# Optimization experiments

Measured on AMD Instinct MI355X. Metric: run time of the kernel, lower is better.

The kernel has to match this reference:

```python
import jax, jax.numpy as jnp
import numpy as np


def _sobel_weights():
    # ImageGradientsLayer: fixed Sobel x/y filters, shape (O=2, I=1, 3, 3)
    gx = jnp.array([[-1., 0., 1.], [-2., 0., 2.], [-1., 0., 1.]], dtype=jnp.float32)
    gy = jnp.array([[-1., -2., -1.], [0., 0., 0.], [1., 2., 1.]], dtype=jnp.float32)
    return jnp.stack([gx, gy])[:, None, :, :]


def _orientation_weights():
    # SIFTOrientationLayer: 8 unit orientation vectors + 2x2 identity, shape (10, 2)
    ratios = jnp.arange(0.125, 2.125, 0.25, dtype=jnp.float32)  # 8 values
    ang = ratios * jnp.pi
    vec = jnp.stack([jnp.cos(ang), jnp.sin(ang)], axis=1)  # (8, 2)
    return jnp.concatenate([vec, jnp.eye(2, dtype=jnp.float32)], axis=0)  # (10, 2)


def setup_inputs() -> dict:
    key = jax.random.key(0)
    x = jax.random.normal(key, (8, 1, 1024, 1024), dtype=jnp.float32)
    return {"x": x, "sobel_w": _sobel_weights(), "orient_w": _orientation_weights()}


def reference(x, sobel_w, orient_w):
    # 1) ImageGradientsLayer: 3x3 Sobel conv, padding=1 -> (B, 2, H, W)
    grads = jax.lax.conv_general_dilated(
        x, sobel_w, window_strides=(1, 1), padding=((1, 1), (1, 1)),
        dimension_numbers=("NCHW", "OIHW", "NCHW"))
    # 2) SIFTOrientationLayer: 1x1 conv == channel projection -> (B, 10, H, W)
    proj = jnp.einsum("bchw,oc->bohw", grads, orient_w)
    # 3) HistogramLayer: one-hot(argmax of orientation dots) * gradient magnitude
    cosines = proj[:, :8]          # (B, 8, H, W)
    im_grads = proj[:, 8:]         # (B, 2, H, W) == grads (identity rows)
    magnitudes = jnp.sqrt(jnp.sum(im_grads * im_grads, axis=1))  # (B, H, W)
    max_idx = jnp.argmax(cosines, axis=1)                        # (B, H, W)
    onehot = jax.nn.one_hot(max_idx, 8, axis=1, dtype=x.dtype)   # (B, 8, H, W)
    hist = onehot * magnitudes[:, None, :, :]
    # 4) SubGridAccumulationLayer: depthwise 4x4 all-ones conv, pad 2 -> (B, 8, H+1, W+1)
    ones_k = jnp.ones((8, 1, 4, 4), dtype=x.dtype)
    out = jax.lax.conv_general_dilated(
        hist, ones_k, window_strides=(1, 1), padding=((2, 2), (2, 2)),
        dimension_numbers=("NCHW", "OIHW", "NCHW"), feature_group_count=8)
    return out
```

## Files before the change

kernel.cpp:

```cpp
#include <hip/hip_runtime.h>
#include <math.h>


#define TWC 61
#define WTH 16
#define WPB 4
#define BTH (WPB*WTH)
#define XC 66
#define XR (BTH+5)
#define PLANE 1050625
#define NCT 17
#define NRT 17

__global__ __launch_bounds__(256, 5)
void sift_fused(const float* __restrict__ x,
                const float* __restrict__ ow,
                float* __restrict__ out)
{
    __shared__ float sx[XR * XC];

    const int tid  = threadIdx.x;
    const int lane = tid & 63;
    const int wv   = tid >> 6;

    const int flat = blockIdx.x + NCT * (blockIdx.y + NRT * blockIdx.z);
    const int bb = flat & 7;
    const int t  = flat >> 3;
    const int bx = t % NCT;
    const int by = t / NCT;

    const int j0 = bx * TWC;
    const int r0 = by * BTH;

    const float* xb = x + (size_t)bb * 1024 * 1024;
    for (int p = tid; p < XR * XC; p += 256) {
        int r = p / XC, c = p - r * XC;
        int gr = r0 - 3 + r, gc = j0 - 3 + c;
        float v = 0.0f;
        if ((unsigned)gr < 1024u && (unsigned)gc < 1024u)
            v = xb[(size_t)gr * 1024 + gc];
        sx[p] = v;
    }
    __syncthreads();

    const int rbase = r0 + WTH * wv;
    if (rbase > 1024) return;

    float wcn[8], wsn[8];
    #pragma unroll
    for (int o = 0; o < 8; ++o) { wcn[o] = ow[2*o]; wsn[o] = ow[2*o+1]; }

    const int gcol = j0 - 2 + lane;
    const bool colok = (unsigned)gcol < 1024u;
    const int gj = j0 + lane;
    const bool canstore = (lane < TWC) && (gj <= 1024);

    float* po[8];
    #pragma unroll
    for (int o = 0; o < 8; ++o) po[o] = out + (size_t)(bb * 8 + o) * PLANE;

    const float* px = sx + (WTH * wv) * XC + lane;
    int hrow = rbase - 2;
    int orow = rbase;
    int vo   = rbase * 1025 + gj;

    float dd0, dd1, dd2, dd3, ww0, ww1, ww2, ww3;
    float cA[8], cB[8], PP0[8], PP1[8], PP2[8], PP3[8];

#define XROWLOAD(DD, WW) { \
    float n0 = px[0], n1 = px[1], n2 = px[2]; px += XC; \
    DD = n2 - n0; \
    WW = n0 + 2.0f*n1 + n2; \
}

#define HSTEP(DT, DM, DB, WT, WB, CP, CC, PR, PC, DOP, DOFIN) { \
    XROWLOAD(DB, WB) \
    float gx = DT + 2.0f*DM + DB; \
    float gy = WB - WT; \
    float msq = gx*gx + gy*gy; \
    float m = (colok && (unsigned)hrow < 1024u) \
                ? __builtin_amdgcn_sqrtf(msq) : 0.0f; \
    hrow++; \
    float pj0 = gx*wcn[0] + gy*wsn[0]; \
    float pj1 = gx*wcn[1] + gy*wsn[1]; \
    float pj2 = gx*wcn[2] + gy*wsn[2]; \
    float pj3 = gx*wcn[3] + gy*wsn[3]; \
    float pj4 = gx*wcn[4] + gy*wsn[4]; \
    float pj5 = gx*wcn[5] + gy*wsn[5]; \
    float pj6 = gx*wcn[6] + gy*wsn[6]; \
    float pj7 = gx*wcn[7] + gy*wsn[7]; \
    bool g01 = pj1 > pj0; float b01 = g01 ? pj1 : pj0; int i01 = g01 ? 1 : 0; \
    bool g23 = pj3 > pj2; float b23 = g23 ? pj3 : pj2; int i23 = g23 ? 3 : 2; \
    bool g45 = pj5 > pj4; float b45 = g45 ? pj5 : pj4; int i45 = g45 ? 5 : 4; \
    bool g67 = pj7 > pj6; float b67 = g67 ? pj7 : pj6; int i67 = g67 ? 7 : 6; \
    bool gA = b23 > b01; float bA = gA ? b23 : b01; int iA = gA ? i23 : i01; \
    bool gB = b67 > b45; float bB = gB ? b67 : b45; int iB = gB ? i67 : i45; \
    int idx = (bB > bA) ? iB : iA; \
    _Pragma("unroll") \
    for (int o = 0; o < 8; ++o) CC[o] = (idx == o) ? m : 0.0f; \
    if (DOP) { \
        _Pragma("unroll") \
        for (int o = 0; o < 8; ++o) PC[o] = CP[o] + CC[o]; \
    } \
    if (DOFIN) { \
        bool ok = canstore && (orow <= 1024); \
        _Pragma("unroll") \
        for (int o = 0; o < 8; ++o) { \
            float v = PR[o] + PC[o]; \
            v += __shfl_down(v, 1); \
            v += __shfl_down(v, 2); \
            if (ok) po[o][vo] = v; \
        } \
        vo += 1025; orow++; \
    } \
}

    XROWLOAD(dd0, ww0)
    XROWLOAD(dd1, ww1)
    HSTEP(dd0, dd1, dd2, ww0, ww2, cA, cB, PP0, PP0, 0, 0)
    HSTEP(dd1, dd2, dd3, ww1, ww3, cB, cA, PP0, PP1, 1, 0)
    HSTEP(dd2, dd3, dd0, ww2, ww0, cA, cB, PP0, PP2, 1, 0)

    #pragma unroll 1
    for (int it = 0; it < 4; ++it) {
        HSTEP(dd3, dd0, dd1, ww3, ww1, cB, cA, PP1, PP3, 1, 1)
        HSTEP(dd0, dd1, dd2, ww0, ww2, cA, cB, PP2, PP0, 1, 1)
        HSTEP(dd1, dd2, dd3, ww1, ww3, cB, cA, PP3, PP1, 1, 1)
        HSTEP(dd2, dd3, dd0, ww2, ww0, cA, cB, PP0, PP2, 1, 1)
    }

#undef HSTEP
#undef XROWLOAD
}

extern "C" void kernel_launch(void* const* d_in, const int* in_sizes, int n_in,
                              void* d_out, int out_size, void* d_ws, size_t ws_size,
                              hipStream_t stream)
{
    const float* x  = (const float*)d_in[0];
    const float* ow = (const float*)d_in[2];
    float* out = (float*)d_out;

    dim3 grid(NCT,
              NRT,
              8);
    sift_fused<<<grid, 256, 0, stream>>>(x, ow, out);
}
```

Before: 90.25 us.

## Process two columns per lane, drop LDS staging, load input directly

Each lane now computes two adjacent output columns, so a block covers 124 columns instead of 61 and fewer column tiles are launched. The shared-memory staging and its barrier are removed; each lane reads four clamped and masked input values per row directly from global memory. The argmax indices are packed into one int, and the 4x4 box sum is built from per-row one-hot magnitudes with fewer shuffles. On even rows the two outputs are written as one float2 store. This trades LDS traffic and sync for redundant global loads through cache, plus higher register pressure (launch bounds lowered to 4).

```diff
diff --git a/kernel.cpp b/kernel.cpp
--- a/kernel.cpp
+++ b/kernel.cpp
@@ -2,23 +2,18 @@
 #include <math.h>
 
 
-#define TWC 61
+#define TWC 124
 #define WTH 16
-#define WPB 4
-#define BTH (WPB*WTH)
-#define XC 66
-#define XR (BTH+5)
+#define BTH 64
+#define NCT 9
+#define NRT 17
 #define PLANE 1050625
-#define NCT 17
-#define NRT 17
 
-__global__ __launch_bounds__(256, 5)
+__global__ __launch_bounds__(256, 4)
 void sift_fused(const float* __restrict__ x,
                 const float* __restrict__ ow,
                 float* __restrict__ out)
 {
-    __shared__ float sx[XR * XC];
-
     const int tid  = threadIdx.x;
     const int lane = tid & 63;
     const int wv   = tid >> 6;
@@ -28,121 +23,173 @@
     const int t  = flat >> 3;
     const int bx = t % NCT;
     const int by = t / NCT;
-
     const int j0 = bx * TWC;
     const int r0 = by * BTH;
 
-    const float* xb = x + (size_t)bb * 1024 * 1024;
-    for (int p = tid; p < XR * XC; p += 256) {
-        int r = p / XC, c = p - r * XC;
-        int gr = r0 - 3 + r, gc = j0 - 3 + c;
-        float v = 0.0f;
-        if ((unsigned)gr < 1024u && (unsigned)gc < 1024u)
-            v = xb[(size_t)gr * 1024 + gc];
-        sx[p] = v;
-    }
-    __syncthreads();
-
     const int rbase = r0 + WTH * wv;
     if (rbase > 1024) return;
+
+    const float* xb = x + (size_t)bb * 1024 * 1024;
 
     float wcn[8], wsn[8];
     #pragma unroll
     for (int o = 0; o < 8; ++o) { wcn[o] = ow[2*o]; wsn[o] = ow[2*o+1]; }
 
-    const int gcol = j0 - 2 + lane;
-    const bool colok = (unsigned)gcol < 1024u;
-    const int gj = j0 + lane;
-    const bool canstore = (lane < TWC) && (gj <= 1024);
+    const int c0 = j0 - 3 + 2 * lane;
+    const int cc0 = min(max(c0    , 0), 1023);
+    const int cc1 = min(max(c0 + 1, 0), 1023);
+    const int cc2 = min(max(c0 + 2, 0), 1023);
+    const int cc3 = min(max(c0 + 3, 0), 1023);
+    const float mk0 = ((unsigned)(c0    ) < 1024u) ? 1.0f : 0.0f;
+    const float mk1 = ((unsigned)(c0 + 1) < 1024u) ? 1.0f : 0.0f;
+    const float mk2 = ((unsigned)(c0 + 2) < 1024u) ? 1.0f : 0.0f;
+    const float mk3 = ((unsigned)(c0 + 3) < 1024u) ? 1.0f : 0.0f;
+
+    const int h0 = j0 - 2 + 2 * lane;
+    const float cm0 = ((unsigned)h0       < 1024u) ? 1.0f : 0.0f;
+    const float cm1 = ((unsigned)(h0 + 1) < 1024u) ? 1.0f : 0.0f;
+
+    const int oc0 = j0 + 2 * lane;
+    const bool st0 = (2 * lane     < TWC) && (oc0     <= 1024);
+    const bool st1 = (2 * lane + 1 < TWC) && (oc0 + 1 <= 1024);
+    const bool stpair  = st0 && st1;
+    const bool st0only = st0 && !st1;
 
     float* po[8];
     #pragma unroll
     for (int o = 0; o < 8; ++o) po[o] = out + (size_t)(bb * 8 + o) * PLANE;
 
-    const float* px = sx + (WTH * wv) * XC + lane;
-    int hrow = rbase - 2;
+    int vo   = rbase * 1025 + oc0;
     int orow = rbase;
-    int vo   = rbase * 1025 + gj;
+    int gr   = rbase - 3;
 
-    float dd0, dd1, dd2, dd3, ww0, ww1, ww2, ww3;
-    float cA[8], cB[8], PP0[8], PP1[8], PP2[8], PP3[8];
+    float q0d0,q0d1,q0w0,q0w1, q1d0,q1d1,q1w0,q1w1;
+    float q2d0,q2d1,q2w0,q2w1, q3d0,q3d1,q3w0,q3w1;
+    float r0m0,r0m1, r1m0,r1m1, r2m0,r2m1, r3m0,r3m1;
+    int   r0ip, r1ip, r2ip, r3ip;
 
-#define XROWLOAD(DD, WW) { \
-    float n0 = px[0], n1 = px[1], n2 = px[2]; px += XC; \
-    DD = n2 - n0; \
-    WW = n0 + 2.0f*n1 + n2; \
+#define XLOAD(BD0,BD1,BW0,BW1) { \
+    float x0_,x1_,x2_,x3_; \
+    if ((unsigned)gr < 1024u) { \
+        const float* rp = xb + ((size_t)(unsigned)gr << 10); \
+        x0_ = rp[cc0]*mk0; x1_ = rp[cc1]*mk1; \
+        x2_ = rp[cc2]*mk2; x3_ = rp[cc3]*mk3; \
+    } else { x0_=0.0f; x1_=0.0f; x2_=0.0f; x3_=0.0f; } \
+    gr++; \
+    BD0 = x2_ - x0_; \
+    BD1 = x3_ - x1_; \
+    BW0 = x0_ + 2.0f*x1_ + x2_; \
+    BW1 = x1_ + 2.0f*x2_ + x3_; \
 }
 
-#define HSTEP(DT, DM, DB, WT, WB, CP, CC, PR, PC, DOP, DOFIN) { \
-    XROWLOAD(DB, WB) \
-    float gx = DT + 2.0f*DM + DB; \
-    float gy = WB - WT; \
-    float msq = gx*gx + gy*gy; \
-    float m = (colok && (unsigned)hrow < 1024u) \
-                ? __builtin_amdgcn_sqrtf(msq) : 0.0f; \
-    hrow++; \
-    float pj0 = gx*wcn[0] + gy*wsn[0]; \
-    float pj1 = gx*wcn[1] + gy*wsn[1]; \
-    float pj2 = gx*wcn[2] + gy*wsn[2]; \
-    float pj3 = gx*wcn[3] + gy*wsn[3]; \
-    float pj4 = gx*wcn[4] + gy*wsn[4]; \
-    float pj5 = gx*wcn[5] + gy*wsn[5]; \
-    float pj6 = gx*wcn[6] + gy*wsn[6]; \
-    float pj7 = gx*wcn[7] + gy*wsn[7]; \
+#define TOURN8(RES, GX, GY) { \
+    float pj0 = (GX)*wcn[0] + (GY)*wsn[0]; \
+    float pj1 = (GX)*wcn[1] + (GY)*wsn[1]; \
+    float pj2 = (GX)*wcn[2] + (GY)*wsn[2]; \
+    float pj3 = (GX)*wcn[3] + (GY)*wsn[3]; \
+    float pj4 = (GX)*wcn[4] + (GY)*wsn[4]; \
+    float pj5 = (GX)*wcn[5] + (GY)*wsn[5]; \
+    float pj6 = (GX)*wcn[6] + (GY)*wsn[6]; \
+    float pj7 = (GX)*wcn[7] + (GY)*wsn[7]; \
     bool g01 = pj1 > pj0; float b01 = g01 ? pj1 : pj0; int i01 = g01 ? 1 : 0; \
     bool g23 = pj3 > pj2; float b23 = g23 ? pj3 : pj2; int i23 = g23 ? 3 : 2; \
     bool g45 = pj5 > pj4; float b45 = g45 ? pj5 : pj4; int i45 = g45 ? 5 : 4; \
     bool g67 = pj7 > pj6; float b67 = g67 ? pj7 : pj6; int i67 = g67 ? 7 : 6; \
     bool gA = b23 > b01; float bA = gA ? b23 : b01; int iA = gA ? i23 : i01; \
     bool gB = b67 > b45; float bB = gB ? b67 : b45; int iB = gB ? i67 : i45; \
-    int idx = (bB > bA) ? iB : iA; \
-    _Pragma("unroll") \
-    for (int o = 0; o < 8; ++o) CC[o] = (idx == o) ? m : 0.0f; \
-    if (DOP) { \
-        _Pragma("unroll") \
-        for (int o = 0; o < 8; ++o) PC[o] = CP[o] + CC[o]; \
-    } \
-    if (DOFIN) { \
-        bool ok = canstore && (orow <= 1024); \
-        _Pragma("unroll") \
-        for (int o = 0; o < 8; ++o) { \
-            float v = PR[o] + PC[o]; \
-            v += __shfl_down(v, 1); \
-            v += __shfl_down(v, 2); \
-            if (ok) po[o][vo] = v; \
-        } \
-        vo += 1025; orow++; \
-    } \
+    RES = (bB > bA) ? iB : iA; \
 }
 
-    XROWLOAD(dd0, ww0)
-    XROWLOAD(dd1, ww1)
-    HSTEP(dd0, dd1, dd2, ww0, ww2, cA, cB, PP0, PP0, 0, 0)
-    HSTEP(dd1, dd2, dd3, ww1, ww3, cB, cA, PP0, PP1, 1, 0)
-    HSTEP(dd2, dd3, dd0, ww2, ww0, cA, cB, PP0, PP2, 1, 0)
+#define HSTEP(TD0,TD1,TW0,TW1, MD0,MD1,MW0,MW1, BD0,BD1,BW0,BW1, RM0,RM1,RIP) { \
+    XLOAD(BD0,BD1,BW0,BW1) \
+    float rowm = ((unsigned)(gr - 3) < 1022u) ? 1.0f : \
+                 (((unsigned)(gr - 2) < 1024u) ? 1.0f : 0.0f); \
+    rowm = ((unsigned)(gr - 2) < 1024u) ? 1.0f : 0.0f; \
+    float gm0 = cm0 * rowm, gm1 = cm1 * rowm; \
+    float gx0 = TD0 + 2.0f*MD0 + BD0; \
+    float gy0 = BW0 - TW0; \
+    float gx1 = TD1 + 2.0f*MD1 + BD1; \
+    float gy1 = BW1 - TW1; \
+    RM0 = __builtin_amdgcn_sqrtf(gx0*gx0 + gy0*gy0) * gm0; \
+    RM1 = __builtin_amdgcn_sqrtf(gx1*gx1 + gy1*gy1) * gm1; \
+    int i0_, i1_; \
+    TOURN8(i0_, gx0, gy0) \
+    TOURN8(i1_, gx1, gy1) \
+    RIP = i0_ | (i1_ << 3); \
+}
+
+#define FIN(EVENK) { \
+    bool rowok = (orow <= 1024); \
+    int e00 = r0ip & 7, e01 = r0ip >> 3; \
+    int e10 = r1ip & 7, e11 = r1ip >> 3; \
+    int e20 = r2ip & 7, e21 = r2ip >> 3; \
+    int e30 = r3ip & 7, e31 = r3ip >> 3; \
+    _Pragma("unroll") \
+    for (int o = 0; o < 8; ++o) { \
+        float a_ = (e00 == o ? r0m0 : 0.0f); \
+        a_ += (e10 == o ? r1m0 : 0.0f); \
+        a_ += (e20 == o ? r2m0 : 0.0f); \
+        a_ += (e30 == o ? r3m0 : 0.0f); \
+        float b_ = (e01 == o ? r0m1 : 0.0f); \
+        b_ += (e11 == o ? r1m1 : 0.0f); \
+        b_ += (e21 == o ? r2m1 : 0.0f); \
+        b_ += (e31 == o ? r3m1 : 0.0f); \
+        float S_ = a_ + b_; \
+        float Sd_ = __shfl_down(S_, 1); \
+        float Ad_ = __shfl_down(a_, 2); \
+        float E_ = S_ + Sd_; \
+        float O_ = b_ + Sd_ + Ad_; \
+        if (EVENK) { \
+            if (rowok && stpair) { \
+                float2 pv; pv.x = E_; pv.y = O_; \
+                *reinterpret_cast<float2*>(po[o] + vo) = pv; \
+            } else if (rowok && st0only) { \
+                po[o][vo] = E_; \
+            } \
+        } else { \
+            if (rowok && st0) po[o][vo] = E_; \
+            if (rowok && st1) po[o][vo + 1] = O_; \
+        } \
+    } \
+    vo += 1025; orow++; \
+}
+
+    XLOAD(q0d0,q0d1,q0w0,q0w1)
+    XLOAD(q1d0,q1d1,q1w0,q1w1)
+    HSTEP(q0d0,q0d1,q0w0,q0w1, q1d0,q1d1,q1w0,q1w1, q2d0,q2d1,q2w0,q2w1,
+          r0m0,r0m1,r0ip)
+    HSTEP(q1d0,q1d1,q1w0,q1w1, q2d0,q2d1,q2w0,q2w1, q3d0,q3d1,q3w0,q3w1,
+          r1m0,r1m1,r1ip)
+    HSTEP(q2d0,q2d1,q2w0,q2w1, q3d0,q3d1,q3w0,q3w1, q0d0,q0d1,q0w0,q0w1,
+          r2m0,r2m1,r2ip)
 
     #pragma unroll 1
     for (int it = 0; it < 4; ++it) {
-        HSTEP(dd3, dd0, dd1, ww3, ww1, cB, cA, PP1, PP3, 1, 1)
-        HSTEP(dd0, dd1, dd2, ww0, ww2, cA, cB, PP2, PP0, 1, 1)
-        HSTEP(dd1, dd2, dd3, ww1, ww3, cB, cA, PP3, PP1, 1, 1)
-        HSTEP(dd2, dd3, dd0, ww2, ww0, cA, cB, PP0, PP2, 1, 1)
+        HSTEP(q3d0,q3d1,q3w0,q3w1, q0d0,q0d1,q0w0,q0w1, q1d0,q1d1,q1w0,q1w1,
+              r3m0,r3m1,r3ip) FIN(1)
+        HSTEP(q0d0,q0d1,q0w0,q0w1, q1d0,q1d1,q1w0,q1w1, q2d0,q2d1,q2w0,q2w1,
+              r0m0,r0m1,r0ip) FIN(0)
+        HSTEP(q1d0,q1d1,q1w0,q1w1, q2d0,q2d1,q2w0,q2w1, q3d0,q3d1,q3w0,q3w1,
+              r1m0,r1m1,r1ip) FIN(1)
+        HSTEP(q2d0,q2d1,q2w0,q2w1, q3d0,q3d1,q3w0,q3w1, q0d0,q0d1,q0w0,q0w1,
+              r2m0,r2m1,r2ip) FIN(0)
     }
 
+#undef FIN
 #undef HSTEP
-#undef XROWLOAD
+#undef TOURN8
+#undef XLOAD
 }
 
 extern "C" void kernel_launch(void* const* d_in, const int* in_sizes, int n_in,
                               void* d_out, int out_size, void* d_ws, size_t ws_size,
                               hipStream_t stream)
 {
+    (void)in_sizes; (void)n_in; (void)d_ws; (void)ws_size; (void)out_size;
     const float* x  = (const float*)d_in[0];
     const float* ow = (const float*)d_in[2];
     float* out = (float*)d_out;
 
-    dim3 grid(NCT,
-              NRT,
-              8);
+    dim3 grid(NCT, NRT, 8);
     sift_fused<<<grid, 256, 0, stream>>>(x, ow, out);
 }
```

After: 121.6 us. 34.8% more time.
